# Optimization experiments

Hardware: AMD Instinct MI355X
Metric: run time of the kernel (lower is better)

Reference implementation:

```python
import jax, jax.numpy as jnp
import numpy as np

N_NODES = 50000
N_EDGES = 600000
N_GRAPHS = 2500
F_IN = 11  # QM9 num_node_features


def setup_inputs() -> dict:
    key = jax.random.key(0)
    ks = jax.random.split(key, 14)
    x = jax.random.normal(ks[0], (N_NODES, F_IN), jnp.float32)
    edge_index = jax.random.randint(ks[1], (2, N_EDGES), 0, N_NODES)
    batch = jnp.sort(jax.random.randint(ks[2], (N_NODES,), 0, N_GRAPHS))

    def lin(k, fan_in, fan_out):
        s = 1.0 / np.sqrt(fan_in)
        return jax.random.uniform(k, (fan_in, fan_out), jnp.float32, -s, s)

    params = dict(
        W1=lin(ks[3], F_IN, 128), b1=jnp.zeros((128,), jnp.float32),
        W2=lin(ks[4], 128, 64),   b2=jnp.zeros((64,), jnp.float32),
        Wf1=lin(ks[5], 64, 128),  bf1=jnp.zeros((128,), jnp.float32),
        Wf2=lin(ks[6], 128, 64),  bf2=jnp.zeros((64,), jnp.float32),
        Wf3=lin(ks[7], 64, 1),    bf3=jnp.zeros((1,), jnp.float32),
    )
    return dict(x=x, edge_index=edge_index, batch=batch, **params)


def reference(x, edge_index, batch, W1, b1, W2, b2, Wf1, bf1, Wf2, bf2, Wf3, bf3):
    N = x.shape[0]
    # --- GCN normalization (PyG gcn_norm): add self-loops, symmetric D^-1/2 A D^-1/2 ---
    self_loop = jnp.arange(N)
    src = jnp.concatenate([edge_index[0], self_loop])  # [E+N]
    dst = jnp.concatenate([edge_index[1], self_loop])
    deg = jax.ops.segment_sum(jnp.ones_like(dst, jnp.float32), dst, num_segments=N)
    dis = jnp.where(deg > 0, jax.lax.rsqrt(jnp.maximum(deg, 1.0)), 0.0)  # deg^-1/2
    norm = dis[src] * dis[dst]  # [E+N]

    def gcn_conv(h, W, b):
        h = h @ W  # transform first (small fan-in)
        msg = h[src] * norm[:, None]  # gather + normalize
        return jax.ops.segment_sum(msg, dst, num_segments=N) + b  # scatter-add

    h = jax.nn.relu(gcn_conv(x, W1, b1))
    h = jax.nn.relu(gcn_conv(h, W2, b2))

    # --- global_mean_pool ---
    sums = jax.ops.segment_sum(h, batch, num_segments=N_GRAPHS)
    cnt = jax.ops.segment_sum(jnp.ones((N,), jnp.float32), batch, num_segments=N_GRAPHS)
    g = sums / jnp.maximum(cnt, 1.0)[:, None]  # [G, 64]

    # --- MLP head ---
    g = jax.nn.relu(g @ Wf1 + bf1)
    g = jax.nn.relu(g @ Wf2 + bf2)
    return g @ Wf3 + bf3  # [G, 1]
```

## Files before the change

### kernel.cpp

```cpp
#include <hip/hip_runtime.h>

#define F0 11
#define F1 128
#define F2 64

__global__ void k_count(const int* __restrict__ dst, int E, int* __restrict__ cnt) {
    int e = blockIdx.x * blockDim.x + threadIdx.x;
    if (e < E) atomicAdd(&cnt[dst[e]], 1);
}

__global__ void k_scanA(const int* __restrict__ deg, int* __restrict__ rowloc,
                        int* __restrict__ bsum, int N) {
    __shared__ int s[256];
    int i = blockIdx.x * 256 + threadIdx.x;
    int v = (i < N) ? deg[i] : 0;
    s[threadIdx.x] = v;
    __syncthreads();
    for (int o = 1; o < 256; o <<= 1) {
        int t = (threadIdx.x >= o) ? s[threadIdx.x - o] : 0;
        __syncthreads();
        s[threadIdx.x] += t;
        __syncthreads();
    }
    if (i < N) rowloc[i] = s[threadIdx.x] - v;
    if (threadIdx.x == 255) bsum[blockIdx.x] = s[255];
}

__global__ void k_scanB(int* __restrict__ bsum, int B) {
    __shared__ int s[256];
    int t = threadIdx.x;
    int v = (t < B) ? bsum[t] : 0;
    s[t] = v;
    __syncthreads();
    for (int o = 1; o < 256; o <<= 1) {
        int u = (t >= o) ? s[t - o] : 0;
        __syncthreads();
        s[t] += u;
        __syncthreads();
    }
    if (t < B) bsum[t] = s[t] - v;
}

__global__ void k_scanC(const int* __restrict__ rowloc, const int* __restrict__ bsum,
                        const int* __restrict__ deg, int* __restrict__ rowptr,
                        float* __restrict__ dis, int N) {
    int i = blockIdx.x * 256 + threadIdx.x;
    if (i < N) {
        rowptr[i] = rowloc[i] + bsum[blockIdx.x];
        dis[i] = 1.0f / sqrtf((float)(deg[i] + 1));
    }
}

__global__ void k_scatter(const int* __restrict__ src, const int* __restrict__ dst,
                          const int* __restrict__ rowptr, int* __restrict__ fill,
                          int* __restrict__ esrc, int E) {
    int e = blockIdx.x * blockDim.x + threadIdx.x;
    if (e >= E) return;
    int d = dst[e];
    int pos = rowptr[d] + atomicAdd(&fill[d], 1);
    esrc[pos] = src[e];
}

__global__ void k_agg1l1(const int* __restrict__ rowptr, const int* __restrict__ deg,
                         const int* __restrict__ esrc, const float* __restrict__ x,
                         const float* __restrict__ dis, const float* __restrict__ W1,
                         const float* __restrict__ b1, float* __restrict__ h1, int N) {
    __shared__ float sW[F0 * F1];
    __shared__ float sb[F1];
    int t = threadIdx.x;
    for (int i = t; i < F0 * F1; i += 256) sW[i] = W1[i];
    if (t < F1) sb[t] = b1[t];
    __syncthreads();

    int wid = t >> 6, lane = t & 63;
    int n = blockIdx.x * 4 + wid;
    if (n >= N) return;

    int r0 = rowptr[n], dn_edges = deg[n];
    int eo = lane >> 4, f = lane & 15;

    float acc = 0.0f;
    for (int j = r0 + eo; j < r0 + dn_edges; j += 4) {
        int s = esrc[j];
        float w = dis[s];
        if (f < F0) acc += x[s * F0 + f] * w;
    }
    acc += __shfl_xor(acc, 16, 64);
    acc += __shfl_xor(acc, 32, 64);

    float dn = dis[n];
    float afull = acc * dn;
    if (f < F0) afull += x[n * F0 + f] * dn * dn;

    float o1 = sb[lane], o2 = sb[lane + 64];
#pragma unroll
    for (int k = 0; k < F0; k++) {
        float ak = __shfl(afull, k, 64);
        o1 += ak * sW[k * F1 + lane];
        o2 += ak * sW[k * F1 + lane + 64];
    }
    h1[(size_t)n * F1 + lane]      = fmaxf(o1, 0.0f);
    h1[(size_t)n * F1 + lane + 64] = fmaxf(o2, 0.0f);
}

__global__ void k_l2(const float* __restrict__ h1, const float* __restrict__ W2,
                     float* __restrict__ t2, int N) {
    __shared__ float sW[F1 * F2];
    __shared__ float sh[4][F1];
    int t = threadIdx.x;
    int grp = t >> 6, lane = t & 63;
    for (int i = t; i < F1 * F2; i += 256) sW[i] = W2[i];
    int n0 = blockIdx.x * 16;
    for (int r = 0; r < 4; r++) {
        int n = n0 + r * 4 + grp;
        __syncthreads();
        if (n < N) {
            sh[grp][lane]      = h1[(size_t)n * F1 + lane];
            sh[grp][lane + 64] = h1[(size_t)n * F1 + lane + 64];
        }
        __syncthreads();
        if (n < N) {
            float acc = 0.0f;
#pragma unroll
            for (int k = 0; k < F1; k++) acc += sh[grp][k] * sW[k * F2 + lane];
            t2[(size_t)n * F2 + lane] = acc;
        }
    }
}

__global__ void k_agg2pool(const int* __restrict__ rowptr, const int* __restrict__ deg,
                           const int* __restrict__ esrc, const float* __restrict__ t2,
                           const float* __restrict__ dis, const float* __restrict__ b2,
                           const int* __restrict__ batch, float* __restrict__ gsum,
                           float* __restrict__ gcnt, int N) {
    int t = threadIdx.x;
    int wid = t >> 6, lane = t & 63;
    int n = blockIdx.x * 4 + wid;
    if (n >= N) return;

    int r0 = rowptr[n], r1 = r0 + deg[n];
    float acc = 0.0f;
    for (int base = r0; base < r1; base += 64) {
        int m = min(64, r1 - base);
        int sidx = 0; float wdis = 0.0f;
        if (lane < m) {
            sidx = esrc[base + lane];
            wdis = dis[sidx];
        }
        for (int j = 0; j < m; j++) {
            int s   = __shfl(sidx, j, 64);
            float w = __shfl(wdis, j, 64);
            acc += w * t2[(size_t)s * F2 + lane];
        }
    }
    float dn = dis[n];
    float h2 = fmaxf(acc * dn + t2[(size_t)n * F2 + lane] * dn * dn + b2[lane], 0.0f);
    int g = batch[n];
    atomicAdd(&gsum[g * F2 + lane], h2);
    if (lane == 0) atomicAdd(&gcnt[g], 1.0f);
}

__global__ void k_head(const float* __restrict__ gsum, const float* __restrict__ gcnt,
                       const float* __restrict__ Wf1, const float* __restrict__ bf1,
                       const float* __restrict__ Wf2, const float* __restrict__ bf2,
                       const float* __restrict__ Wf3, const float* __restrict__ bf3,
                       float* __restrict__ out, int G) {
    __shared__ float sg[F2];
    __shared__ float sh1[F1];
    __shared__ float sh2[F2];
    int g = blockIdx.x, t = threadIdx.x;
    if (t < F2) {
        float c = fmaxf(gcnt[g], 1.0f);
        sg[t] = gsum[g * F2 + t] / c;
    }
    __syncthreads();
    {
        float a = bf1[t];
#pragma unroll 8
        for (int k = 0; k < F2; k++) a += sg[k] * Wf1[k * F1 + t];
        sh1[t] = fmaxf(a, 0.0f);
    }
    __syncthreads();
    if (t < F2) {
        float a = bf2[t];
#pragma unroll 8
        for (int k = 0; k < F1; k++) a += sh1[k] * Wf2[k * F2 + t];
        sh2[t] = fmaxf(a, 0.0f);
    }
    __syncthreads();
    if (t < F2) {
        float v = sh2[t] * Wf3[t];
        for (int off = 32; off > 0; off >>= 1) v += __shfl_down(v, off, 64);
        if (t == 0) out[g] = v + bf3[0];
    }
}

extern "C" void kernel_launch(void* const* d_in, const int* in_sizes, int n_in,
                              void* d_out, int out_size, void* d_ws, size_t ws_size,
                              hipStream_t stream) {
    const float* x     = (const float*)d_in[0];
    const int*   ei    = (const int*)d_in[1];
    const int*   batch = (const int*)d_in[2];
    const float* W1    = (const float*)d_in[3];
    const float* b1    = (const float*)d_in[4];
    const float* W2    = (const float*)d_in[5];
    const float* b2    = (const float*)d_in[6];
    const float* Wf1   = (const float*)d_in[7];
    const float* bf1   = (const float*)d_in[8];
    const float* Wf2   = (const float*)d_in[9];
    const float* bf2   = (const float*)d_in[10];
    const float* Wf3   = (const float*)d_in[11];
    const float* bf3   = (const float*)d_in[12];
    float* out = (float*)d_out;

    const int N = in_sizes[0] / F0;
    const int E = in_sizes[1] / 2;
    const int G = out_size;
    const int* src = ei;
    const int* dst = ei + E;

    size_t off = 0;
    auto carve = [&](size_t bytes) {
        void* p = (char*)d_ws + off;
        off += (bytes + 255) & ~(size_t)255;
        return p;
    };
    int*   deg    = (int*)  carve((size_t)N * 4);
    int*   rowloc = (int*)  carve((size_t)N * 4);
    int*   rowptr = (int*)  carve((size_t)N * 4);
    int*   fill   = (int*)  carve((size_t)N * 4);
    int*   bsum   = (int*)  carve(256 * 4);
    float* dis    = (float*)carve((size_t)N * 4);
    int*   esrc   = (int*)  carve((size_t)E * 4);
    float* h1     = (float*)carve((size_t)N * F1 * 4);
    float* t2     = (float*)carve((size_t)N * F2 * 4);
    float* gsum   = (float*)carve((size_t)G * F2 * 4);
    float* gcnt   = (float*)carve((size_t)G * 4);
    (void)ws_size; (void)n_in;

    const int NB = (N + 255) / 256;

    hipMemsetAsync(deg,  0, (size_t)N * 4, stream);
    hipMemsetAsync(fill, 0, (size_t)N * 4, stream);
    hipMemsetAsync(gsum, 0, (size_t)G * F2 * 4, stream);
    hipMemsetAsync(gcnt, 0, (size_t)G * 4, stream);

    k_count  <<<(E + 255) / 256, 256, 0, stream>>>(dst, E, deg);
    k_scanA  <<<NB, 256, 0, stream>>>(deg, rowloc, bsum, N);
    k_scanB  <<<1, 256, 0, stream>>>(bsum, NB);
    k_scanC  <<<NB, 256, 0, stream>>>(rowloc, bsum, deg, rowptr, dis, N);
    k_scatter<<<(E + 255) / 256, 256, 0, stream>>>(src, dst, rowptr, fill, esrc, E);
    k_agg1l1 <<<(N + 3) / 4, 256, 0, stream>>>(rowptr, deg, esrc, x, dis, W1, b1, h1, N);
    k_l2     <<<(N + 15) / 16, 256, 0, stream>>>(h1, W2, t2, N);
    k_agg2pool<<<(N + 3) / 4, 256, 0, stream>>>(rowptr, deg, esrc, t2, dis, b2, batch, gsum, gcnt, N);
    k_head   <<<G, F1, 0, stream>>>(gsum, gcnt, Wf1, bf1, Wf2, bf2, Wf3, bf3, out, G);
}
```

Before: 310.4 us.

## Pack edge weights into CSR, register-resident W2, unrolled gather loops

The scatter now writes (src, dis[src]) pairs into a packed int2 CSR array, so the aggregation kernels no longer do a dependent gather of dis per edge. A cursor array initialised from rowptr replaces the separate fill array and its memset, and gsum and gcnt share one allocation cleared by a single memset. The layer-2 transform keeps each lane's W2 column in 128 registers and reads h1 rows as float4 in a grid-stride loop over a fixed grid, replacing the shared-memory version. Both aggregation loops are unrolled with multiple accumulators and prefetching to expose more memory-level parallelism. The costs are twice the edge-array traffic and high register pressure in the layer-2 kernel.

```diff
diff --git a/kernel.cpp b/kernel.cpp
--- a/kernel.cpp
+++ b/kernel.cpp
@@ -43,26 +43,28 @@
 
 __global__ void k_scanC(const int* __restrict__ rowloc, const int* __restrict__ bsum,
                         const int* __restrict__ deg, int* __restrict__ rowptr,
-                        float* __restrict__ dis, int N) {
+                        int* __restrict__ cursor, float* __restrict__ dis, int N) {
     int i = blockIdx.x * 256 + threadIdx.x;
     if (i < N) {
-        rowptr[i] = rowloc[i] + bsum[blockIdx.x];
+        int r = rowloc[i] + bsum[blockIdx.x];
+        rowptr[i] = r;
+        cursor[i] = r;
         dis[i] = 1.0f / sqrtf((float)(deg[i] + 1));
     }
 }
 
 __global__ void k_scatter(const int* __restrict__ src, const int* __restrict__ dst,
-                          const int* __restrict__ rowptr, int* __restrict__ fill,
-                          int* __restrict__ esrc, int E) {
+                          const float* __restrict__ dis, int* __restrict__ cursor,
+                          int2* __restrict__ epack, int E) {
     int e = blockIdx.x * blockDim.x + threadIdx.x;
     if (e >= E) return;
-    int d = dst[e];
-    int pos = rowptr[d] + atomicAdd(&fill[d], 1);
-    esrc[pos] = src[e];
+    int s = src[e], d = dst[e];
+    int pos = atomicAdd(&cursor[d], 1);
+    epack[pos] = make_int2(s, __float_as_int(dis[s]));
 }
 
 __global__ void k_agg1l1(const int* __restrict__ rowptr, const int* __restrict__ deg,
-                         const int* __restrict__ esrc, const float* __restrict__ x,
+                         const int2* __restrict__ epack, const float* __restrict__ x,
                          const float* __restrict__ dis, const float* __restrict__ W1,
                          const float* __restrict__ b1, float* __restrict__ h1, int N) {
     __shared__ float sW[F0 * F1];
@@ -76,14 +78,22 @@
     int n = blockIdx.x * 4 + wid;
     if (n >= N) return;
 
-    int r0 = rowptr[n], dn_edges = deg[n];
+    int r0 = rowptr[n], r1 = r0 + deg[n];
     int eo = lane >> 4, f = lane & 15;
 
     float acc = 0.0f;
-    for (int j = r0 + eo; j < r0 + dn_edges; j += 4) {
-        int s = esrc[j];
-        float w = dis[s];
-        if (f < F0) acc += x[s * F0 + f] * w;
+    int j = r0 + eo;
+    for (; j + 4 < r1; j += 8) {
+        int2 p = epack[j];
+        int2 q = epack[j + 4];
+        if (f < F0) {
+            acc += x[p.x * F0 + f] * __int_as_float(p.y);
+            acc += x[q.x * F0 + f] * __int_as_float(q.y);
+        }
+    }
+    if (j < r1) {
+        int2 p = epack[j];
+        if (f < F0) acc += x[p.x * F0 + f] * __int_as_float(p.y);
     }
     acc += __shfl_xor(acc, 16, 64);
     acc += __shfl_xor(acc, 32, 64);
@@ -103,33 +113,29 @@
     h1[(size_t)n * F1 + lane + 64] = fmaxf(o2, 0.0f);
 }
 
-__global__ void k_l2(const float* __restrict__ h1, const float* __restrict__ W2,
-                     float* __restrict__ t2, int N) {
-    __shared__ float sW[F1 * F2];
-    __shared__ float sh[4][F1];
-    int t = threadIdx.x;
-    int grp = t >> 6, lane = t & 63;
-    for (int i = t; i < F1 * F2; i += 256) sW[i] = W2[i];
-    int n0 = blockIdx.x * 16;
-    for (int r = 0; r < 4; r++) {
-        int n = n0 + r * 4 + grp;
-        __syncthreads();
-        if (n < N) {
-            sh[grp][lane]      = h1[(size_t)n * F1 + lane];
-            sh[grp][lane + 64] = h1[(size_t)n * F1 + lane + 64];
+__global__ void k_l2reg(const float* __restrict__ h1, const float* __restrict__ W2,
+                        float* __restrict__ t2, int N, int nwaves) {
+    int t = threadIdx.x;
+    int lane = t & 63;
+    float w[F1];
+#pragma unroll
+    for (int k = 0; k < F1; k++) w[k] = W2[k * F2 + lane];
+    int wg = blockIdx.x * 4 + (t >> 6);
+    for (int n = wg; n < N; n += nwaves) {
+        const float4* hp = (const float4*)(h1 + (size_t)n * F1);
+        float tv = 0.0f;
+#pragma unroll
+        for (int q = 0; q < F1 / 4; q++) {
+            float4 h4 = hp[q];
+            tv += h4.x * w[4 * q] + h4.y * w[4 * q + 1] +
+                  h4.z * w[4 * q + 2] + h4.w * w[4 * q + 3];
         }
-        __syncthreads();
-        if (n < N) {
-            float acc = 0.0f;
-#pragma unroll
-            for (int k = 0; k < F1; k++) acc += sh[grp][k] * sW[k * F2 + lane];
-            t2[(size_t)n * F2 + lane] = acc;
-        }
+        t2[(size_t)n * F2 + lane] = tv;
     }
 }
 
 __global__ void k_agg2pool(const int* __restrict__ rowptr, const int* __restrict__ deg,
-                           const int* __restrict__ esrc, const float* __restrict__ t2,
+                           const int2* __restrict__ epack, const float* __restrict__ t2,
                            const float* __restrict__ dis, const float* __restrict__ b2,
                            const int* __restrict__ batch, float* __restrict__ gsum,
                            float* __restrict__ gcnt, int N) {
@@ -139,24 +145,34 @@
     if (n >= N) return;
 
     int r0 = rowptr[n], r1 = r0 + deg[n];
-    float acc = 0.0f;
-    for (int base = r0; base < r1; base += 64) {
-        int m = min(64, r1 - base);
-        int sidx = 0; float wdis = 0.0f;
-        if (lane < m) {
-            sidx = esrc[base + lane];
-            wdis = dis[sidx];
+    float a0 = 0.f, a1 = 0.f, a2 = 0.f, a3 = 0.f;
+    int j = r0;
+    if (r1 - r0 >= 4) {
+        int2 p0 = epack[j], p1 = epack[j + 1], p2 = epack[j + 2], p3 = epack[j + 3];
+        j += 4;
+        while (j + 4 <= r1) {
+            int2 q0 = epack[j], q1 = epack[j + 1], q2 = epack[j + 2], q3 = epack[j + 3];
+            a0 += __int_as_float(p0.y) * t2[(size_t)p0.x * F2 + lane];
+            a1 += __int_as_float(p1.y) * t2[(size_t)p1.x * F2 + lane];
+            a2 += __int_as_float(p2.y) * t2[(size_t)p2.x * F2 + lane];
+            a3 += __int_as_float(p3.y) * t2[(size_t)p3.x * F2 + lane];
+            p0 = q0; p1 = q1; p2 = q2; p3 = q3;
+            j += 4;
         }
-        for (int j = 0; j < m; j++) {
-            int s   = __shfl(sidx, j, 64);
-            float w = __shfl(wdis, j, 64);
-            acc += w * t2[(size_t)s * F2 + lane];
-        }
-    }
+        a0 += __int_as_float(p0.y) * t2[(size_t)p0.x * F2 + lane];
+        a1 += __int_as_float(p1.y) * t2[(size_t)p1.x * F2 + lane];
+        a2 += __int_as_float(p2.y) * t2[(size_t)p2.x * F2 + lane];
+        a3 += __int_as_float(p3.y) * t2[(size_t)p3.x * F2 + lane];
+    }
+    for (; j < r1; j++) {
+        int2 p = epack[j];
+        a0 += __int_as_float(p.y) * t2[(size_t)p.x * F2 + lane];
+    }
+    float acc = (a0 + a1) + (a2 + a3);
     float dn = dis[n];
     float h2 = fmaxf(acc * dn + t2[(size_t)n * F2 + lane] * dn * dn + b2[lane], 0.0f);
     int g = batch[n];
-    atomicAdd(&gsum[g * F2 + lane], h2);
+    atomicAdd(&gsum[(size_t)g * F2 + lane], h2);
     if (lane == 0) atomicAdd(&gcnt[g], 1.0f);
 }
 
@@ -228,30 +244,28 @@
     int*   deg    = (int*)  carve((size_t)N * 4);
     int*   rowloc = (int*)  carve((size_t)N * 4);
     int*   rowptr = (int*)  carve((size_t)N * 4);
-    int*   fill   = (int*)  carve((size_t)N * 4);
+    int*   cursor = (int*)  carve((size_t)N * 4);
     int*   bsum   = (int*)  carve(256 * 4);
     float* dis    = (float*)carve((size_t)N * 4);
-    int*   esrc   = (int*)  carve((size_t)E * 4);
+    int2*  epack  = (int2*) carve((size_t)E * 8);
     float* h1     = (float*)carve((size_t)N * F1 * 4);
     float* t2     = (float*)carve((size_t)N * F2 * 4);
-    float* gsum   = (float*)carve((size_t)G * F2 * 4);
-    float* gcnt   = (float*)carve((size_t)G * 4);
+    float* gsum   = (float*)carve((size_t)G * (F2 + 1) * 4);
+    float* gcnt   = gsum + (size_t)G * F2;
     (void)ws_size; (void)n_in;
 
     const int NB = (N + 255) / 256;
 
     hipMemsetAsync(deg,  0, (size_t)N * 4, stream);
-    hipMemsetAsync(fill, 0, (size_t)N * 4, stream);
-    hipMemsetAsync(gsum, 0, (size_t)G * F2 * 4, stream);
-    hipMemsetAsync(gcnt, 0, (size_t)G * 4, stream);
+    hipMemsetAsync(gsum, 0, (size_t)G * (F2 + 1) * 4, stream);
 
     k_count  <<<(E + 255) / 256, 256, 0, stream>>>(dst, E, deg);
     k_scanA  <<<NB, 256, 0, stream>>>(deg, rowloc, bsum, N);
     k_scanB  <<<1, 256, 0, stream>>>(bsum, NB);
-    k_scanC  <<<NB, 256, 0, stream>>>(rowloc, bsum, deg, rowptr, dis, N);
-    k_scatter<<<(E + 255) / 256, 256, 0, stream>>>(src, dst, rowptr, fill, esrc, E);
-    k_agg1l1 <<<(N + 3) / 4, 256, 0, stream>>>(rowptr, deg, esrc, x, dis, W1, b1, h1, N);
-    k_l2     <<<(N + 15) / 16, 256, 0, stream>>>(h1, W2, t2, N);
-    k_agg2pool<<<(N + 3) / 4, 256, 0, stream>>>(rowptr, deg, esrc, t2, dis, b2, batch, gsum, gcnt, N);
+    k_scanC  <<<NB, 256, 0, stream>>>(rowloc, bsum, deg, rowptr, cursor, dis, N);
+    k_scatter<<<(E + 255) / 256, 256, 0, stream>>>(src, dst, dis, cursor, epack, E);
+    k_agg1l1 <<<(N + 3) / 4, 256, 0, stream>>>(rowptr, deg, epack, x, dis, W1, b1, h1, N);
+    k_l2reg  <<<768, 256, 0, stream>>>(h1, W2, t2, N, 768 * 4);
+    k_agg2pool<<<(N + 3) / 4, 256, 0, stream>>>(rowptr, deg, epack, t2, dis, b2, batch, gsum, gcnt, N);
     k_head   <<<G, F1, 0, stream>>>(gsum, gcnt, Wf1, bf1, Wf2, bf2, Wf3, bf3, out, G);
 }
```

Result: slower. 803.4 us (+158.8%).
